# Kernel optimization log

Measured on AMD Instinct MI355X. Metric: run time of the kernel, lower is better.

## Reference

```python
import jax, jax.numpy as jnp
import numpy as np

N_NODES = 50000
N_EDGES = 800000
HID = 256
OUT = 128
NEG_SLOPE = 0.2


def gat_layer(x, src, dst, W_src, W_dst, a_src_vec, a_dst_vec, bias, n_nodes):
    # Dense projections (PyG lin_src / lin_dst for tuple in_channels)
    h_src = x @ W_src              # [N, C]
    h_dst = x @ W_dst              # [N, C]
    # Per-node attention logits (att_src/att_dst dot products)
    a_src = h_src @ a_src_vec      # [N]
    a_dst = h_dst @ a_dst_vec      # [N]
    # Edge logits + LeakyReLU
    e = jax.nn.leaky_relu(a_src[src] + a_dst[dst], NEG_SLOPE)  # [E]
    # Segment softmax over incoming edges of each dst node
    m = jax.ops.segment_max(e, dst, num_segments=n_nodes)      # [N]
    m = jnp.where(jnp.isfinite(m), m, 0.0)                      # empty segments
    ex = jnp.exp(e - m[dst])                                    # [E]
    s = jax.ops.segment_sum(ex, dst, num_segments=n_nodes)     # [N]
    alpha = ex / (s[dst] + 1e-16)                               # [E]
    # Attention-weighted message aggregation (scatter-add to dst)
    msg = alpha[:, None] * h_src[src]                           # [E, C]
    out = jax.ops.segment_sum(msg, dst, num_segments=n_nodes)  # [N, C]
    return out + bias


def setup_inputs() -> dict:
    key = jax.random.key(0)
    ks = jax.random.split(key, 12)
    x = jax.random.normal(ks[0], (N_NODES, HID), dtype=jnp.float32)
    edge_index = jax.random.randint(ks[1], (2, N_EDGES), 0, N_NODES, dtype=jnp.int64)
    sc1 = 1.0 / np.sqrt(HID)
    sc2 = 1.0 / np.sqrt(HID)
    return {
        "x": x,
        "edge_index": edge_index,
        "W1_src": jax.random.normal(ks[2], (HID, HID), dtype=jnp.float32) * sc1,
        "W1_dst": jax.random.normal(ks[3], (HID, HID), dtype=jnp.float32) * sc1,
        "att1_src": jax.random.normal(ks[4], (HID,), dtype=jnp.float32) * sc1,
        "att1_dst": jax.random.normal(ks[5], (HID,), dtype=jnp.float32) * sc1,
        "b1": jnp.zeros((HID,), dtype=jnp.float32),
        "W2_src": jax.random.normal(ks[6], (HID, OUT), dtype=jnp.float32) * sc2,
        "W2_dst": jax.random.normal(ks[7], (HID, OUT), dtype=jnp.float32) * sc2,
        "att2_src": jax.random.normal(ks[8], (OUT,), dtype=jnp.float32) * (1.0 / np.sqrt(OUT)),
        "att2_dst": jax.random.normal(ks[9], (OUT,), dtype=jnp.float32) * (1.0 / np.sqrt(OUT)),
        "b2": jnp.zeros((OUT,), dtype=jnp.float32),
    }


def reference(x, edge_index, W1_src, W1_dst, att1_src, att1_dst, b1,
              W2_src, W2_dst, att2_src, att2_dst, b2):
    src, dst = edge_index[0], edge_index[1]
    h = gat_layer(x, src, dst, W1_src, W1_dst, att1_src, att1_dst, b1, N_NODES)
    h = jax.nn.relu(h)
    out = gat_layer(h, src, dst, W2_src, W2_dst, att2_src, att2_dst, b2, N_NODES)
    return out
```

## Files before the change

### kernel.cpp

```cpp
#include <hip/hip_runtime.h>
#include <math.h>

#define N_NODES 50000
#define N_EDGES 800000
#define HID 256
#define OUT_C 128
#define NEG_SLOPE 0.2f
#define SCAN_NB ((N_NODES + 255) / 256)

typedef __attribute__((ext_vector_type(8))) short bf16x8;
typedef __attribute__((ext_vector_type(4))) float f32x4;
typedef _Float16 half_t;
typedef __attribute__((ext_vector_type(8))) _Float16 half8;

__device__ inline unsigned short bf16_rne(float x) {
    unsigned u = __float_as_uint(x);
    return (unsigned short)((u + 0x7fffu + ((u >> 16) & 1u)) >> 16);
}


__global__ __launch_bounds__(256) void hist_rank_kernel(
    const int* __restrict__ dst, int* __restrict__ counts, int* __restrict__ rank) {
    int e = blockIdx.x * 256 + threadIdx.x;
    if (e < N_EDGES) rank[e] = atomicAdd(&counts[dst[e]], 1);
}

__global__ __launch_bounds__(256) void block_scan_kernel(
    const int* __restrict__ counts, int* __restrict__ excl,
    int* __restrict__ blockSums, int n) {
    __shared__ int waveSums[4];
    int i = blockIdx.x * 256 + threadIdx.x;
    int lane = threadIdx.x & 63;
    int wv = threadIdx.x >> 6;
    int c = (i < n) ? counts[i] : 0;
    int v = c;
    #pragma unroll
    for (int off = 1; off < 64; off <<= 1) {
        int t = __shfl_up(v, off);
        if (lane >= off) v += t;
    }
    if (lane == 63) waveSums[wv] = v;
    __syncthreads();
    int waveOff = 0;
    #pragma unroll
    for (int w = 0; w < 4; w++)
        if (w < wv) waveOff += waveSums[w];
    if (i < n) excl[i] = waveOff + v - c;
    if (threadIdx.x == 255) blockSums[blockIdx.x] = waveOff + v;
}

__global__ __launch_bounds__(256) void add_offsets_kernel(
    int* __restrict__ excl, const int* __restrict__ blockSums, int n) {
    __shared__ int lds[4];
    int tid = threadIdx.x;
    int partial = 0;
    for (int j = tid; j < (int)blockIdx.x; j += 256) partial += blockSums[j];
    #pragma unroll
    for (int off = 32; off > 0; off >>= 1) partial += __shfl_down(partial, off);
    if ((tid & 63) == 0) lds[tid >> 6] = partial;
    __syncthreads();
    int prefix = lds[0] + lds[1] + lds[2] + lds[3];
    int i = blockIdx.x * 256 + tid;
    if (i < n) excl[i] += prefix;
    if (i == 0) excl[n] = N_EDGES;
}


__global__ __launch_bounds__(256) void edge_weight_kernel(
    const int* __restrict__ src, const int* __restrict__ dst,
    const int* __restrict__ offsets, const int* __restrict__ rank,
    const float* __restrict__ a_src, const float* __restrict__ a_dst,
    int2* __restrict__ ew) {
    int e = blockIdx.x * 256 + threadIdx.x;
    if (e >= N_EDGES) return;
    int s = src[e], d = dst[e];
    float l = a_src[s] + a_dst[d];
    l = fmaxf(l, l * NEG_SLOPE);
    float w = __expf(l);
    ew[offsets[d] + rank[e]] = make_int2(s, __float_as_int(w));
}


__global__ __launch_bounds__(64) void compute_v_all_kernel(
    const float* __restrict__ W1s, const float* __restrict__ att1s,
    const float* __restrict__ W1d, const float* __restrict__ att1d,
    const float* __restrict__ W2s, const float* __restrict__ att2s,
    const float* __restrict__ W2d, const float* __restrict__ att2d,
    float* __restrict__ v1s, float* __restrict__ v1d,
    float* __restrict__ v2s, float* __restrict__ v2d) {
    int k = blockIdx.x;
    int lane = threadIdx.x;
    const float* W; const float* att; float* v; int cout;
    switch (blockIdx.y) {
        case 0: W = W1s; att = att1s; v = v1s; cout = HID; break;
        case 1: W = W1d; att = att1d; v = v1d; cout = HID; break;
        case 2: W = W2s; att = att2s; v = v2s; cout = OUT_C; break;
        default: W = W2d; att = att2d; v = v2d; cout = OUT_C; break;
    }
    float sum = 0.f;
    for (int j = lane; j < cout; j += 64)
        sum += W[k * cout + j] * att[j];
    #pragma unroll
    for (int off = 32; off > 0; off >>= 1)
        sum += __shfl_down(sum, off);
    if (lane == 0) v[k] = sum;
}


#define PACK1_T (8 * 17 * 64)
#define PACK2_T (8 * 9 * 64)

__global__ __launch_bounds__(256) void pack_all_kernel(
    const float* __restrict__ W1, const float* __restrict__ v1s, const float* __restrict__ v1d,
    const float* __restrict__ W2, const float* __restrict__ v2s, const float* __restrict__ v2d,
    unsigned short* __restrict__ hi1, unsigned short* __restrict__ lo1,
    unsigned short* __restrict__ hi2, unsigned short* __restrict__ lo2) {
    int t = blockIdx.x * 256 + threadIdx.x;
    const float *W, *vs, *vd; unsigned short *hi, *lo; int cout, NTL, tt;
    if (t < PACK1_T)            { tt = t;           W = W1; vs = v1s; vd = v1d; hi = hi1; lo = lo1; cout = HID;  NTL = 17; }
    else if (t < PACK1_T + PACK2_T) { tt = t - PACK1_T; W = W2; vs = v2s; vd = v2d; hi = hi2; lo = lo2; cout = OUT_C; NTL = 9; }
    else return;
    int lane = tt & 63;
    int tile = (tt >> 6) % NTL;
    int ks = tt / (64 * NTL);
    int m = lane & 15;
    int kbase = ks * 32 + (lane >> 4) * 8;
    #pragma unroll
    for (int j = 0; j < 8; j++) {
        float val;
        if (tile < NTL - 1) val = W[(kbase + j) * cout + tile * 16 + m];
        else val = (m == 0) ? vs[kbase + j] : (m == 1) ? vd[kbase + j] : 0.f;
        unsigned short h = bf16_rne(val);
        hi[tt * 8 + j] = h;
        lo[tt * 8 + j] = bf16_rne(val - __uint_as_float((unsigned)h << 16));
    }
}


template <int COUT, int NT, bool WRITE_A>
__device__ __forceinline__ void gemm_body(
    const float* __restrict__ A, const unsigned short* __restrict__ Bhi,
    const unsigned short* __restrict__ Blo, half_t* __restrict__ H,
    float* __restrict__ a_s, float* __restrict__ a_d, int M, int tile0) {
    const int NTL = COUT / 16 + 1;
    int wave = threadIdx.x >> 6, lane = threadIdx.x & 63;
    int m = lane & 15, quad = lane >> 4;
    int row0 = blockIdx.x * 128 + wave * 32;
    f32x4 acc[2][NT];
    #pragma unroll
    for (int rg = 0; rg < 2; rg++)
        #pragma unroll
        for (int nt = 0; nt < NT; nt++)
            acc[rg][nt] = (f32x4){0.f, 0.f, 0.f, 0.f};

    const float* arow[2];
    #pragma unroll
    for (int rg = 0; rg < 2; rg++) {
        int r = row0 + rg * 16 + m;
        if (r >= M) r = M - 1;
        arow[rg] = A + (size_t)r * HID;
    }

    for (int ks = 0; ks < 8; ks++) {
        bf16x8 ah[2], al[2];
        #pragma unroll
        for (int rg = 0; rg < 2; rg++) {
            const float* ap = arow[rg] + ks * 32 + quad * 8;
            float4 v0 = *(const float4*)ap;
            float4 v1 = *(const float4*)(ap + 4);
            float av[8] = {v0.x, v0.y, v0.z, v0.w, v1.x, v1.y, v1.z, v1.w};
            #pragma unroll
            for (int j = 0; j < 8; j++) {
                unsigned short h = bf16_rne(av[j]);
                float hf = __uint_as_float((unsigned)h << 16);
                ah[rg][j] = (short)h;
                al[rg][j] = (short)bf16_rne(av[j] - hf);
            }
        }
        #pragma unroll
        for (int nt = 0; nt < NT; nt++) {
            int tile = (WRITE_A && nt == NT - 1) ? (COUT / 16) : (tile0 + nt);
            size_t fbase = ((size_t)(ks * NTL + tile) * 64 + lane) * 8;
            bf16x8 bh = *(const bf16x8*)(Bhi + fbase);
            bf16x8 bl = *(const bf16x8*)(Blo + fbase);
            acc[0][nt] = __builtin_amdgcn_mfma_f32_16x16x32_bf16(ah[0], bh, acc[0][nt], 0, 0, 0);
            acc[1][nt] = __builtin_amdgcn_mfma_f32_16x16x32_bf16(ah[1], bh, acc[1][nt], 0, 0, 0);
            acc[0][nt] = __builtin_amdgcn_mfma_f32_16x16x32_bf16(ah[0], bl, acc[0][nt], 0, 0, 0);
            acc[1][nt] = __builtin_amdgcn_mfma_f32_16x16x32_bf16(ah[1], bl, acc[1][nt], 0, 0, 0);
            acc[0][nt] = __builtin_amdgcn_mfma_f32_16x16x32_bf16(al[0], bh, acc[0][nt], 0, 0, 0);
            acc[1][nt] = __builtin_amdgcn_mfma_f32_16x16x32_bf16(al[1], bh, acc[1][nt], 0, 0, 0);
        }
    }
    const int NW = WRITE_A ? NT - 1 : NT;
    #pragma unroll
    for (int rg = 0; rg < 2; rg++)
        #pragma unroll
        for (int nt = 0; nt < NW; nt++)
            #pragma unroll
            for (int r = 0; r < 4; r++) {
                int row = row0 + rg * 16 + quad * 4 + r;
                if (row < M)
                    H[(size_t)row * COUT + (tile0 + nt) * 16 + m] = (half_t)acc[rg][nt][r];
            }
    if (WRITE_A) {
        #pragma unroll
        for (int rg = 0; rg < 2; rg++)
            #pragma unroll
            for (int r = 0; r < 4; r++) {
                int row = row0 + rg * 16 + quad * 4 + r;
                if (row < M) {
                    if (m == 0) a_s[row] = acc[rg][NT - 1][r];
                    else if (m == 1) a_d[row] = acc[rg][NT - 1][r];
                }
            }
    }
}

template <int COUT>
__global__ __launch_bounds__(256) void mfma_gemm_a_kernel(
    const float* __restrict__ A, const unsigned short* __restrict__ Bhi,
    const unsigned short* __restrict__ Blo, half_t* __restrict__ H,
    float* __restrict__ a_s, float* __restrict__ a_d, int M) {
    if (blockIdx.y == 0)
        gemm_body<COUT, 9, true>(A, Bhi, Blo, H, a_s, a_d, M, 0);
    else
        gemm_body<COUT, 8, false>(A, Bhi, Blo, H, a_s, a_d, M, 8);
}


template <int C, bool RELU>
__global__ __launch_bounds__(256) void fused_aggregate_kernel(
    const int* __restrict__ offsets, const int2* __restrict__ ew,
    const half_t* __restrict__ h, const float* __restrict__ bias,
    float* __restrict__ out) {
    constexpr int CH = 16;
    constexpr int G = (C == 256) ? 32 : 16;
    constexpr int NPW = 64 / G;
    int wid = blockIdx.x * 4 + (threadIdx.x >> 6);
    int lane = threadIdx.x & 63;
    int sub = lane / G;
    int gl = lane & (G - 1);
    int node = wid * NPW + sub;
    if (node >= N_NODES) return;
    int beg = offsets[node], end = offsets[node + 1];
    float ssum = 0.f;
    float acc[8];
    #pragma unroll
    for (int k = 0; k < 8; k++) acc[k] = 0.f;
    unsigned c0 = (unsigned)gl * 8u;

    for (int base = beg; base < end; base += CH) {
        int cnt = end - base; if (cnt > CH) cnt = CH;
        int li = gl & (CH - 1);
        int eidx = base + ((li < cnt) ? li : 0);
        int2 ev = ew[eidx];
        int idxs[CH]; float w[CH];
        #pragma unroll
        for (int j = 0; j < CH; j++) {
            idxs[j] = __shfl(ev.x, j, G);
            float wv = __int_as_float(__shfl(ev.y, j, G));
            w[j] = (j < cnt) ? wv : 0.f;
        }
        half8 hv[CH];
        #pragma unroll
        for (int j = 0; j < CH; j++)
            hv[j] = *(const half8*)(h + ((size_t)(unsigned)idxs[j] * C + c0));
        #pragma unroll
        for (int j = 0; j < CH; j++) {
            ssum += w[j];
            #pragma unroll
            for (int k = 0; k < 8; k++)
                acc[k] += w[j] * (float)hv[j][k];
        }
    }

    float inv = 1.f / (ssum + 1e-16f);
    float4 bv0 = *(const float4*)(bias + c0);
    float4 bv1 = *(const float4*)(bias + c0 + 4);
    float o[8];
    o[0] = acc[0] * inv + bv0.x; o[1] = acc[1] * inv + bv0.y;
    o[2] = acc[2] * inv + bv0.z; o[3] = acc[3] * inv + bv0.w;
    o[4] = acc[4] * inv + bv1.x; o[5] = acc[5] * inv + bv1.y;
    o[6] = acc[6] * inv + bv1.z; o[7] = acc[7] * inv + bv1.w;
    if (RELU) {
        #pragma unroll
        for (int k = 0; k < 8; k++) o[k] = fmaxf(o[k], 0.f);
    }
    float* op = out + (size_t)node * C + c0;
    *(float4*)op       = make_float4(o[0], o[1], o[2], o[3]);
    *(float4*)(op + 4) = make_float4(o[4], o[5], o[6], o[7]);
}

extern "C" void kernel_launch(void* const* d_in, const int* in_sizes, int n_in,
                              void* d_out, int out_size, void* d_ws, size_t ws_size,
                              hipStream_t stream) {
    const float* x     = (const float*)d_in[0];
    const int*   edge  = (const int*)d_in[1];
    const int*   src   = edge;
    const int*   dst   = edge + N_EDGES;
    const float* W1s   = (const float*)d_in[2];
    const float* W1d   = (const float*)d_in[3];
    const float* att1s = (const float*)d_in[4];
    const float* att1d = (const float*)d_in[5];
    const float* b1    = (const float*)d_in[6];
    const float* W2s   = (const float*)d_in[7];
    const float* W2d   = (const float*)d_in[8];
    const float* att2s = (const float*)d_in[9];
    const float* att2d = (const float*)d_in[10];
    const float* b2    = (const float*)d_in[11];
    float* out = (float*)d_out;

    float* ws    = (float*)d_ws;
    half_t* h1   = (half_t*)ws;
    int2* ew     = (int2*)(ws + (size_t)N_NODES * HID / 2);
    float* act2  = ws + (size_t)N_NODES * HID;
    float* a_s   = act2 + (size_t)N_NODES * HID;
    float* a_d   = a_s + N_NODES;
    float* vbuf  = a_d + N_NODES;
    int* ibase      = (int*)(vbuf + 4 * HID);
    int* rank       = ibase;
    int* counts     = rank + N_EDGES;
    int* offsets    = counts + N_NODES;
    int* blockSums  = offsets + N_NODES + 1;
    unsigned short* wp1h = (unsigned short*)(((uintptr_t)(blockSums + SCAN_NB) + 15) & ~(uintptr_t)15);
    unsigned short* wp1l = wp1h + PACK1_T * 8;
    unsigned short* wp2h = wp1l + PACK1_T * 8;
    unsigned short* wp2l = wp2h + PACK2_T * 8;
    float* v1s = vbuf, *v1d = vbuf + HID, *v2s = vbuf + 2 * HID, *v2d = vbuf + 3 * HID;
    half_t* h2 = h1;

    const int edgeBlocks = (N_EDGES + 255) / 256;
    const int gemmBlocks = (N_NODES + 127) / 128;
    const int aggBlocks1 = ((N_NODES + 1) / 2 + 3) / 4;
    const int aggBlocks2 = ((N_NODES + 3) / 4 + 3) / 4;

    hipMemsetAsync(counts, 0, N_NODES * sizeof(int), stream);
    hist_rank_kernel<<<edgeBlocks, 256, 0, stream>>>(dst, counts, rank);
    block_scan_kernel<<<SCAN_NB, 256, 0, stream>>>(counts, offsets, blockSums, N_NODES);
    add_offsets_kernel<<<SCAN_NB, 256, 0, stream>>>(offsets, blockSums, N_NODES);

    compute_v_all_kernel<<<dim3(HID, 4), 64, 0, stream>>>(
        W1s, att1s, W1d, att1d, W2s, att2s, W2d, att2d, v1s, v1d, v2s, v2d);
    pack_all_kernel<<<(PACK1_T + PACK2_T + 255) / 256, 256, 0, stream>>>(
        W1s, v1s, v1d, W2s, v2s, v2d, wp1h, wp1l, wp2h, wp2l);

    mfma_gemm_a_kernel<HID><<<dim3(gemmBlocks, 2), 256, 0, stream>>>(
        x, wp1h, wp1l, h1, a_s, a_d, N_NODES);
    edge_weight_kernel<<<edgeBlocks, 256, 0, stream>>>(
        src, dst, offsets, rank, a_s, a_d, ew);
    fused_aggregate_kernel<HID, true><<<aggBlocks1, 256, 0, stream>>>(
        offsets, ew, h1, b1, act2);

    mfma_gemm_a_kernel<OUT_C><<<dim3(gemmBlocks, 1), 256, 0, stream>>>(
        act2, wp2h, wp2l, h2, a_s, a_d, N_NODES);
    edge_weight_kernel<<<edgeBlocks, 256, 0, stream>>>(
        src, dst, offsets, rank, a_s, a_d, ew);
    fused_aggregate_kernel<OUT_C, false><<<aggBlocks2, 256, 0, stream>>>(
        offsets, ew, h2, b2, out);
}
```

Measured before the change: 364.4 us.

## Partition aggregation by channel slices mapped to XCDs for L2 locality

The aggregation kernel now splits the feature channels into slices of 32 and assigns each slice to one XCD via blockIdx modulo 8. Each lane group of 8 handles 4 channels per node, so every XCD's L2 only needs to cache its own column slice of the gathered h rows. The intent is to cut cross-XCD duplication of the gathered features in L2. In exchange, each edge's index and weight is reloaded by eight blocks, and each gather is narrower (8-byte half4 loads instead of 16-byte loads).

```diff
diff --git a/kernel.cpp b/kernel.cpp
--- a/kernel.cpp
+++ b/kernel.cpp
@@ -11,7 +11,7 @@
 typedef __attribute__((ext_vector_type(8))) short bf16x8;
 typedef __attribute__((ext_vector_type(4))) float f32x4;
 typedef _Float16 half_t;
-typedef __attribute__((ext_vector_type(8))) _Float16 half8;
+typedef __attribute__((ext_vector_type(4))) _Float16 half4;
 
 __device__ inline unsigned short bf16_rne(float x) {
     unsigned u = __float_as_uint(x);
@@ -234,61 +234,63 @@
     const half_t* __restrict__ h, const float* __restrict__ bias,
     float* __restrict__ out) {
     constexpr int CH = 16;
-    constexpr int G = (C == 256) ? 32 : 16;
-    constexpr int NPW = 64 / G;
-    int wid = blockIdx.x * 4 + (threadIdx.x >> 6);
-    int lane = threadIdx.x & 63;
-    int sub = lane / G;
-    int gl = lane & (G - 1);
-    int node = wid * NPW + sub;
-    if (node >= N_NODES) return;
+    constexpr int G = 8;
+    constexpr int NPB = 32;
+    int bx = blockIdx.x;
+    int xcd = bx & 7;
+    int nb = bx >> 3;
+    int slice, nodeBase, nodeLim;
+    if (C == 256) { slice = xcd; nodeBase = 0; nodeLim = N_NODES; }
+    else { slice = xcd & 3; nodeBase = (xcd >> 2) * (N_NODES / 2); nodeLim = nodeBase + N_NODES / 2; }
+    int wave = threadIdx.x >> 6, lane = threadIdx.x & 63;
+    int sub = lane >> 3, gl = lane & 7;
+    int node = nodeBase + nb * NPB + wave * 8 + sub;
+    if (node >= nodeLim) return;
     int beg = offsets[node], end = offsets[node + 1];
-    float ssum = 0.f;
-    float acc[8];
-    #pragma unroll
-    for (int k = 0; k < 8; k++) acc[k] = 0.f;
-    unsigned c0 = (unsigned)gl * 8u;
+    int c0 = slice * 32 + gl * 4;
+    const half_t* hs = h + c0;
+    float acc0 = 0.f, acc1 = 0.f, acc2 = 0.f, acc3 = 0.f, ssum = 0.f;
 
     for (int base = beg; base < end; base += CH) {
         int cnt = end - base; if (cnt > CH) cnt = CH;
-        int li = gl & (CH - 1);
-        int eidx = base + ((li < cnt) ? li : 0);
-        int2 ev = ew[eidx];
+        int2 ev0 = ew[base + ((gl < cnt) ? gl : 0)];
+        int2 ev1 = ew[base + ((gl + 8 < cnt) ? gl + 8 : 0)];
         int idxs[CH]; float w[CH];
         #pragma unroll
-        for (int j = 0; j < CH; j++) {
-            idxs[j] = __shfl(ev.x, j, G);
-            float wv = __int_as_float(__shfl(ev.y, j, G));
+        for (int j = 0; j < 8; j++) {
+            idxs[j] = __shfl(ev0.x, j, G);
+            float wv = __int_as_float(__shfl(ev0.y, j, G));
             w[j] = (j < cnt) ? wv : 0.f;
         }
-        half8 hv[CH];
+        #pragma unroll
+        for (int j = 0; j < 8; j++) {
+            idxs[8 + j] = __shfl(ev1.x, j, G);
+            float wv = __int_as_float(__shfl(ev1.y, j, G));
+            w[8 + j] = (8 + j < cnt) ? wv : 0.f;
+        }
+        half4 hv[CH];
         #pragma unroll
         for (int j = 0; j < CH; j++)
-            hv[j] = *(const half8*)(h + ((size_t)(unsigned)idxs[j] * C + c0));
+            hv[j] = *(const half4*)(hs + (size_t)(unsigned)idxs[j] * C);
         #pragma unroll
         for (int j = 0; j < CH; j++) {
             ssum += w[j];
-            #pragma unroll
-            for (int k = 0; k < 8; k++)
-                acc[k] += w[j] * (float)hv[j][k];
+            acc0 += w[j] * (float)hv[j][0];
+            acc1 += w[j] * (float)hv[j][1];
+            acc2 += w[j] * (float)hv[j][2];
+            acc3 += w[j] * (float)hv[j][3];
         }
     }
 
     float inv = 1.f / (ssum + 1e-16f);
-    float4 bv0 = *(const float4*)(bias + c0);
-    float4 bv1 = *(const float4*)(bias + c0 + 4);
-    float o[8];
-    o[0] = acc[0] * inv + bv0.x; o[1] = acc[1] * inv + bv0.y;
-    o[2] = acc[2] * inv + bv0.z; o[3] = acc[3] * inv + bv0.w;
-    o[4] = acc[4] * inv + bv1.x; o[5] = acc[5] * inv + bv1.y;
-    o[6] = acc[6] * inv + bv1.z; o[7] = acc[7] * inv + bv1.w;
+    float4 bv = *(const float4*)(bias + c0);
+    float o0 = acc0 * inv + bv.x, o1 = acc1 * inv + bv.y;
+    float o2 = acc2 * inv + bv.z, o3 = acc3 * inv + bv.w;
     if (RELU) {
-        #pragma unroll
-        for (int k = 0; k < 8; k++) o[k] = fmaxf(o[k], 0.f);
-    }
-    float* op = out + (size_t)node * C + c0;
-    *(float4*)op       = make_float4(o[0], o[1], o[2], o[3]);
-    *(float4*)(op + 4) = make_float4(o[4], o[5], o[6], o[7]);
+        o0 = fmaxf(o0, 0.f); o1 = fmaxf(o1, 0.f);
+        o2 = fmaxf(o2, 0.f); o3 = fmaxf(o3, 0.f);
+    }
+    *(float4*)(out + (size_t)node * C + c0) = make_float4(o0, o1, o2, o3);
 }
 
 extern "C" void kernel_launch(void* const* d_in, const int* in_sizes, int n_in,
@@ -331,8 +333,8 @@
 
     const int edgeBlocks = (N_EDGES + 255) / 256;
     const int gemmBlocks = (N_NODES + 127) / 128;
-    const int aggBlocks1 = ((N_NODES + 1) / 2 + 3) / 4;
-    const int aggBlocks2 = ((N_NODES + 3) / 4 + 3) / 4;
+    const int aggBlocks1 = 8 * ((N_NODES + 31) / 32);
+    const int aggBlocks2 = 8 * ((N_NODES / 2 + 31) / 32);
 
     hipMemsetAsync(counts, 0, N_NODES * sizeof(int), stream);
     hist_rank_kernel<<<edgeBlocks, 256, 0, stream>>>(dst, counts, rank);
```

Measured after the change: 376.8 us. 1.03x slower.
